# Kernel tuning notes

Measured on AMD Instinct MI355X. Metric: run time of the kernel, lower is better.

Reference implementation:

```python
import jax, jax.numpy as jnp
import numpy as np

B, N, D = 256, 512, 64  # batch, positions, channels; units = spatial_units = D


def setup_inputs() -> dict:
    key = jax.random.key(0)
    ks = jax.random.split(key, 9)
    g = 1.0 / np.sqrt(D)  # glorot-ish scale for square matrices
    return {
        "x": jax.random.normal(ks[0], (B, N, D), dtype=jnp.float32),
        "Wq_t": jax.random.normal(ks[1], (D, D), dtype=jnp.float32) * g,
        "Wk_t": jax.random.normal(ks[2], (D, D), dtype=jnp.float32) * g,
        "Wv_t": jax.random.normal(ks[3], (D, D), dtype=jnp.float32) * g,
        "Wq_s": jax.random.normal(ks[4], (D, D), dtype=jnp.float32) * g,
        "Wk_s": jax.random.normal(ks[5], (D, D), dtype=jnp.float32) * g,
        "Wv_s": jax.random.normal(ks[6], (D, D), dtype=jnp.float32) * g,
        "Wd_t": jax.random.normal(ks[7], (D, D), dtype=jnp.float32) * g,
        "bd_t": jnp.zeros((D,), dtype=jnp.float32),
        "Wd_s": jax.random.normal(ks[8], (D, D), dtype=jnp.float32) * g,
        "bd_s": jnp.zeros((D,), dtype=jnp.float32),
    }


def _branch(x, Wq, Wk, Wv, Wd, bd):
    # x: [B, N, D]; one self-attention branch followed by a Dense layer.
    q = jnp.einsum("bnd,de->bne", x, Wq)
    k = jnp.einsum("bnd,de->bne", x, Wk)
    v = jnp.einsum("bnd,de->bne", x, Wv)
    scale = 1.0 / jnp.sqrt(jnp.asarray(Wk.shape[-1], dtype=x.dtype))
    scores = jnp.einsum("bne,bme->bnm", q, k) * scale  # [B, N, N]
    w = jax.nn.softmax(scores, axis=-1)
    attn = jnp.einsum("bnm,bmd->bnd", w, v)
    return jnp.einsum("bnd,de->bne", attn, Wd) + bd


def reference(x, Wq_t, Wk_t, Wv_t, Wq_s, Wk_s, Wv_s, Wd_t, bd_t, Wd_s, bd_s):
    temporal = _branch(x, Wq_t, Wk_t, Wv_t, Wd_t, bd_t)
    spatial = _branch(x, Wq_s, Wk_s, Wv_s, Wd_s, bd_s)
    gate = jax.nn.sigmoid(temporal + spatial)
    return x * gate
```

## Files before the change

kernel.cpp:

```cpp
#include <hip/hip_runtime.h>
#include <hip/hip_bf16.h>

typedef __attribute__((ext_vector_type(8))) short short8;
typedef __attribute__((ext_vector_type(4))) short short4v;
typedef __attribute__((ext_vector_type(4))) float float4v;

#define MFMA16(a, b, c) __builtin_amdgcn_mfma_f32_16x16x32_bf16((a), (b), (c), 0, 0, 0)
#define LDS_FENCE() asm volatile("" ::: "memory")

constexpr int kN = 512;
constexpr int kD = 64;
constexpr int kThreads = 1024;

constexpr int LDS_TOTAL_BYTES = 79872 * 2;

static __device__ __forceinline__ unsigned short f2bf(float f) {
  unsigned int u = __float_as_uint(f);
  u = (u + 0x7fffu + ((u >> 16) & 1u)) >> 16;
  return (unsigned short)u;
}

static __device__ __forceinline__ unsigned int f2bf2(float a, float b) {
  union {
    __hip_bfloat162 h;
    unsigned int u;
  } cvt;
  cvt.h = __float22bfloat162_rn(float2{a, b});
  return cvt.u;
}

union S8U4 {
  short8 s8;
  unsigned int u4[4];
};

__global__ __launch_bounds__(kThreads, 4) void ts_attn_fused(
    const float* __restrict__ x, const float* __restrict__ Wq_t,
    const float* __restrict__ Wk_t, const float* __restrict__ Wv_t,
    const float* __restrict__ Wq_s, const float* __restrict__ Wk_s,
    const float* __restrict__ Wv_s, const float* __restrict__ Wd_t,
    const float* __restrict__ bd_t, const float* __restrict__ Wd_s,
    const float* __restrict__ bd_s, float* __restrict__ out) {
  extern __shared__ __align__(16) unsigned short smem_us[];
  unsigned short* Ksw = smem_us;
  unsigned short* Vsw = smem_us + 32768;
  unsigned short* Wdsw = smem_us + 65536;
  unsigned short* rep = smem_us + 69632;

  const int tid = threadIdx.x;
  const int wv = tid >> 6;
  const int lane = tid & 63;
  const int ln = lane & 15;
  const int quad = lane >> 4;
  const int b = blockIdx.x;

  const float* xb = x + (size_t)b * (kN * kD);
  float* outb = out + (size_t)b * (kN * kD);

  const int sd = tid >> 4;
  const int se0 = (tid & 15) * 4;
  const int sbase = (sd >> 3) * 512 + (sd & 7);

  float bdsum[4];
#pragma unroll
  for (int nt = 0; nt < 4; ++nt) bdsum[nt] = bd_t[nt * 16 + ln] + bd_s[nt * 16 + ln];

#pragma unroll 1
  for (int br = 0; br < 2; ++br) {
    const float* Wq = br ? Wq_s : Wq_t;
    const float* Wk = br ? Wk_s : Wk_t;
    const float* Wv = br ? Wv_s : Wv_t;
    const float* Wd = br ? Wd_s : Wd_t;

    {
      const float* srcs[3] = {Wq, Wk, Wv};
      unsigned short* dsts[3] = {rep, rep + 4096, Wdsw};
#pragma unroll
      for (int g = 0; g < 3; ++g) {
        const float4v u = *reinterpret_cast<const float4v*>(srcs[g] + sd * 64 + se0);
        unsigned short* dst = dsts[g];
#pragma unroll
        for (int i = 0; i < 4; ++i) dst[sbase + (se0 + i) * 8] = f2bf(u[i]);
      }
    }
    __syncthreads();

    short8 xa[2][2];
#pragma unroll
    for (int mi = 0; mi < 2; ++mi) {
      const int mrow = (wv + mi * 16) * 16 + ln;
      const float4v u0 = *reinterpret_cast<const float4v*>(xb + mrow * 64 + quad * 8);
      const float4v v0 = *reinterpret_cast<const float4v*>(xb + mrow * 64 + quad * 8 + 4);
      const float4v u1 = *reinterpret_cast<const float4v*>(xb + mrow * 64 + 32 + quad * 8);
      const float4v v1 = *reinterpret_cast<const float4v*>(xb + mrow * 64 + 32 + quad * 8 + 4);
      S8U4 t0, t1;
      t0.u4[0] = f2bf2(u0[0], u0[1]);
      t0.u4[1] = f2bf2(u0[2], u0[3]);
      t0.u4[2] = f2bf2(v0[0], v0[1]);
      t0.u4[3] = f2bf2(v0[2], v0[3]);
      t1.u4[0] = f2bf2(u1[0], u1[1]);
      t1.u4[1] = f2bf2(u1[2], u1[3]);
      t1.u4[2] = f2bf2(v1[0], v1[1]);
      t1.u4[3] = f2bf2(v1[2], v1[3]);
      xa[mi][0] = t0.s8;
      xa[mi][1] = t1.s8;
    }

    short4v qd[2][4];
#pragma unroll
    for (int g = 0; g < 3; ++g) {
      const unsigned short* Wl = (g == 0) ? rep : (g == 1) ? (rep + 4096) : Wdsw;
#pragma unroll
      for (int nt = 0; nt < 4; ++nt) {
        const short8 b0 = *reinterpret_cast<const short8*>(Wl + quad * 512 + (nt * 16 + ln) * 8);
        const short8 b1 =
            *reinterpret_cast<const short8*>(Wl + (4 + quad) * 512 + (nt * 16 + ln) * 8);
#pragma unroll
        for (int mi = 0; mi < 2; ++mi) {
          const int mt = wv + mi * 16;
          float4v acc = {0.f, 0.f, 0.f, 0.f};
          acc = MFMA16(xa[mi][0], b0, acc);
          acc = MFMA16(xa[mi][1], b1, acc);
          if (g == 0) {
            short4v pk;
#pragma unroll
            for (int r = 0; r < 4; ++r) pk[r] = (short)f2bf(acc[r]);
            qd[mi][nt] = pk;
          } else if (g == 1) {
            const int ehi = nt * 2 + (ln >> 3);
            const int elo = ln & 7;
#pragma unroll
            for (int r = 0; r < 4; ++r)
              Ksw[ehi * 4096 + (mt * 16 + quad * 4 + r) * 8 + elo] = f2bf(acc[r]);
          } else {
            short4v pk;
#pragma unroll
            for (int r = 0; r < 4; ++r) pk[r] = (short)f2bf(acc[r]);
            const int vbase = (mt * 2 + (quad >> 1)) * 512 + (nt * 16 + ln) * 8 + (quad & 1) * 4;
            *reinterpret_cast<short4v*>(Vsw + vbase) = pk;
          }
        }
      }
    }
    __syncthreads();

    {
      const float4v u = *reinterpret_cast<const float4v*>(Wd + sd * 64 + se0);
#pragma unroll
      for (int i = 0; i < 4; ++i) Wdsw[sbase + (se0 + i) * 8] = f2bf(u[i]);
    }
    __syncthreads();

    unsigned short* buf = rep + wv * 640;

    short8 q[2][2];
#pragma unroll
    for (int u = 0; u < 2; ++u) {
#pragma unroll
      for (int p = 0; p < 2; ++p) {
#pragma unroll
        for (int h = 0; h < 2; ++h)
#pragma unroll
          for (int r = 0; r < 4; ++r)
            buf[(quad * 4 + r) * 40 + h * 16 + ln] = (unsigned short)qd[u][p * 2 + h][r];
        LDS_FENCE();
        q[u][p] = *reinterpret_cast<const short8*>(buf + ln * 40 + quad * 8);
        LDS_FENCE();
      }
    }

    float sum[2][4];
    float4v o[2][4];
#pragma unroll
    for (int u = 0; u < 2; ++u)
#pragma unroll
      for (int i = 0; i < 4; ++i) {
        sum[u][i] = 0.f;
        o[u][i] = (float4v){0.f, 0.f, 0.f, 0.f};
      }

#pragma unroll 1
    for (int sc = 0; sc < 8; ++sc) {
      float4v s[2][4];
#pragma unroll
      for (int t = 0; t < 4; ++t) {
        const int nt = sc * 4 + t;
        const short8 k0 = *reinterpret_cast<const short8*>(Ksw + quad * 4096 + (nt * 16 + ln) * 8);
        const short8 k1 =
            *reinterpret_cast<const short8*>(Ksw + (4 + quad) * 4096 + (nt * 16 + ln) * 8);
#pragma unroll
        for (int u = 0; u < 2; ++u) {
          float4v acc = {0.f, 0.f, 0.f, 0.f};
          acc = MFMA16(q[u][0], k0, acc);
          acc = MFMA16(q[u][1], k1, acc);
          s[u][t] = acc;
        }
      }
#pragma unroll
      for (int kc2 = 0; kc2 < 2; ++kc2) {
        const int kcg = sc * 2 + kc2;
        short8 pa[2];
#pragma unroll
        for (int u = 0; u < 2; ++u) {
#pragma unroll
          for (int t2 = 0; t2 < 2; ++t2) {
            const float4v sv = s[u][kc2 * 2 + t2];
#pragma unroll
            for (int r = 0; r < 4; ++r) {
              const float p = __expf(sv[r] * 0.125f);
              sum[u][r] += p;
              buf[(quad * 4 + r) * 40 + t2 * 16 + ln] = f2bf(p);
            }
          }
          LDS_FENCE();
          pa[u] = *reinterpret_cast<const short8*>(buf + ln * 40 + quad * 8);
          LDS_FENCE();
        }
#pragma unroll
        for (int nto = 0; nto < 4; ++nto) {
          const short8 vf =
              *reinterpret_cast<const short8*>(Vsw + (kcg * 4 + quad) * 512 + (nto * 16 + ln) * 8);
          o[0][nto] = MFMA16(pa[0], vf, o[0][nto]);
          o[1][nto] = MFMA16(pa[1], vf, o[1][nto]);
        }
      }
    }

#pragma unroll
    for (int dd = 1; dd < 16; dd <<= 1)
#pragma unroll
      for (int u = 0; u < 2; ++u)
#pragma unroll
        for (int r = 0; r < 4; ++r) sum[u][r] += __shfl_xor(sum[u][r], dd, 64);
    float inv[2][4];
#pragma unroll
    for (int u = 0; u < 2; ++u)
#pragma unroll
      for (int r = 0; r < 4; ++r) inv[u][r] = 1.0f / sum[u][r];

    short8 a[2][2];
#pragma unroll
    for (int u = 0; u < 2; ++u) {
#pragma unroll
      for (int p = 0; p < 2; ++p) {
#pragma unroll
        for (int h = 0; h < 2; ++h)
#pragma unroll
          for (int r = 0; r < 4; ++r)
            buf[(quad * 4 + r) * 40 + h * 16 + ln] = f2bf(o[u][p * 2 + h][r] * inv[u][r]);
        LDS_FENCE();
        a[u][p] = *reinterpret_cast<const short8*>(buf + ln * 40 + quad * 8);
        LDS_FENCE();
      }
    }

#pragma unroll
    for (int nt = 0; nt < 4; ++nt) {
      const short8 w0 = *reinterpret_cast<const short8*>(Wdsw + quad * 512 + (nt * 16 + ln) * 8);
      const short8 w1 =
          *reinterpret_cast<const short8*>(Wdsw + (4 + quad) * 512 + (nt * 16 + ln) * 8);
      const int col = nt * 16 + ln;
#pragma unroll
      for (int u = 0; u < 2; ++u) {
        float4v d4 = {0.f, 0.f, 0.f, 0.f};
        d4 = MFMA16(a[u][0], w0, d4);
        d4 = MFMA16(a[u][1], w1, d4);
        const int m0 = (wv + u * 16) * 16 + quad * 4;
        if (br == 0) {
#pragma unroll
          for (int r = 0; r < 4; ++r) outb[(m0 + r) * 64 + col] = d4[r];
        } else {
#pragma unroll
          for (int r = 0; r < 4; ++r) {
            const float z = outb[(m0 + r) * 64 + col] + d4[r] + bdsum[nt];
            const float gate = 1.0f / (1.0f + __expf(-z));
            outb[(m0 + r) * 64 + col] = xb[(m0 + r) * 64 + col] * gate;
          }
        }
      }
    }
    __syncthreads();
  }
}

extern "C" void kernel_launch(void* const* d_in, const int* in_sizes, int n_in,
                              void* d_out, int out_size, void* d_ws, size_t ws_size,
                              hipStream_t stream) {
  const float* x = (const float*)d_in[0];
  const float* Wq_t = (const float*)d_in[1];
  const float* Wk_t = (const float*)d_in[2];
  const float* Wv_t = (const float*)d_in[3];
  const float* Wq_s = (const float*)d_in[4];
  const float* Wk_s = (const float*)d_in[5];
  const float* Wv_s = (const float*)d_in[6];
  const float* Wd_t = (const float*)d_in[7];
  const float* bd_t = (const float*)d_in[8];
  const float* Wd_s = (const float*)d_in[9];
  const float* bd_s = (const float*)d_in[10];
  float* out = (float*)d_out;

  hipFuncSetAttribute(reinterpret_cast<const void*>(ts_attn_fused),
                      hipFuncAttributeMaxDynamicSharedMemorySize, LDS_TOTAL_BYTES);
  ts_attn_fused<<<dim3(256), dim3(kThreads), LDS_TOTAL_BYTES, stream>>>(
      x, Wq_t, Wk_t, Wv_t, Wq_s, Wk_s, Wv_s, Wd_t, bd_t, Wd_s, bd_s, out);
}
```

Before: 211.5 us.

## Halve block to 8 waves, each computing four query tiles with shared K/V fragments

The block drops from 16 to 8 waves, so each wave now owns four 16-row query tiles instead of two. Each K and V fragment read from LDS is reused across twice as many MFMAs, which cuts LDS read traffic per unit of work. The per-wave staging buffer becomes two slots so that transposes can be batched, and the x-load is moved ahead of the barrier. In exchange, register pressure roughly doubles for the accumulators and there is less parallelism per block, with launch bounds lowered to match.

```diff
diff --git a/kernel.cpp b/kernel.cpp
--- a/kernel.cpp
+++ b/kernel.cpp
@@ -10,7 +10,7 @@
 
 constexpr int kN = 512;
 constexpr int kD = 64;
-constexpr int kThreads = 1024;
+constexpr int kThreads = 512;
 
 constexpr int LDS_TOTAL_BYTES = 79872 * 2;
 
@@ -34,7 +34,7 @@
   unsigned int u4[4];
 };
 
-__global__ __launch_bounds__(kThreads, 4) void ts_attn_fused(
+__global__ __launch_bounds__(kThreads, 2) void ts_attn_fused(
     const float* __restrict__ x, const float* __restrict__ Wq_t,
     const float* __restrict__ Wk_t, const float* __restrict__ Wv_t,
     const float* __restrict__ Wq_s, const float* __restrict__ Wk_s,
@@ -57,13 +57,16 @@
   const float* xb = x + (size_t)b * (kN * kD);
   float* outb = out + (size_t)b * (kN * kD);
 
-  const int sd = tid >> 4;
-  const int se0 = (tid & 15) * 4;
+  const int sd = tid >> 3;
+  const int se0 = (tid & 7) * 8;
   const int sbase = (sd >> 3) * 512 + (sd & 7);
 
   float bdsum[4];
 #pragma unroll
   for (int nt = 0; nt < 4; ++nt) bdsum[nt] = bd_t[nt * 16 + ln] + bd_s[nt * 16 + ln];
+
+  unsigned short* slot0 = rep + wv * 1280;
+  unsigned short* slot1 = slot0 + 640;
 
 #pragma unroll 1
   for (int br = 0; br < 2; ++br) {
@@ -77,18 +80,20 @@
       unsigned short* dsts[3] = {rep, rep + 4096, Wdsw};
 #pragma unroll
       for (int g = 0; g < 3; ++g) {
-        const float4v u = *reinterpret_cast<const float4v*>(srcs[g] + sd * 64 + se0);
+        const float4v u0 = *reinterpret_cast<const float4v*>(srcs[g] + sd * 64 + se0);
+        const float4v u1 = *reinterpret_cast<const float4v*>(srcs[g] + sd * 64 + se0 + 4);
         unsigned short* dst = dsts[g];
 #pragma unroll
-        for (int i = 0; i < 4; ++i) dst[sbase + (se0 + i) * 8] = f2bf(u[i]);
-      }
-    }
-    __syncthreads();
-
-    short8 xa[2][2];
-#pragma unroll
-    for (int mi = 0; mi < 2; ++mi) {
-      const int mrow = (wv + mi * 16) * 16 + ln;
+        for (int i = 0; i < 4; ++i) dst[sbase + (se0 + i) * 8] = f2bf(u0[i]);
+#pragma unroll
+        for (int i = 0; i < 4; ++i) dst[sbase + (se0 + 4 + i) * 8] = f2bf(u1[i]);
+      }
+    }
+
+    short8 xa[4][2];
+#pragma unroll
+    for (int mi = 0; mi < 4; ++mi) {
+      const int mrow = (wv + mi * 8) * 16 + ln;
       const float4v u0 = *reinterpret_cast<const float4v*>(xb + mrow * 64 + quad * 8);
       const float4v v0 = *reinterpret_cast<const float4v*>(xb + mrow * 64 + quad * 8 + 4);
       const float4v u1 = *reinterpret_cast<const float4v*>(xb + mrow * 64 + 32 + quad * 8);
@@ -105,8 +110,9 @@
       xa[mi][0] = t0.s8;
       xa[mi][1] = t1.s8;
     }
-
-    short4v qd[2][4];
+    __syncthreads();
+
+    short4v qd[4][4];
 #pragma unroll
     for (int g = 0; g < 3; ++g) {
       const unsigned short* Wl = (g == 0) ? rep : (g == 1) ? (rep + 4096) : Wdsw;
@@ -116,8 +122,8 @@
         const short8 b1 =
             *reinterpret_cast<const short8*>(Wl + (4 + quad) * 512 + (nt * 16 + ln) * 8);
 #pragma unroll
-        for (int mi = 0; mi < 2; ++mi) {
-          const int mt = wv + mi * 16;
+        for (int mi = 0; mi < 4; ++mi) {
+          const int mt = wv + mi * 8;
           float4v acc = {0.f, 0.f, 0.f, 0.f};
           acc = MFMA16(xa[mi][0], b0, acc);
           acc = MFMA16(xa[mi][1], b1, acc);
@@ -145,34 +151,35 @@
     __syncthreads();
 
     {
-      const float4v u = *reinterpret_cast<const float4v*>(Wd + sd * 64 + se0);
-#pragma unroll
-      for (int i = 0; i < 4; ++i) Wdsw[sbase + (se0 + i) * 8] = f2bf(u[i]);
+      const float4v u0 = *reinterpret_cast<const float4v*>(Wd + sd * 64 + se0);
+      const float4v u1 = *reinterpret_cast<const float4v*>(Wd + sd * 64 + se0 + 4);
+#pragma unroll
+      for (int i = 0; i < 4; ++i) Wdsw[sbase + (se0 + i) * 8] = f2bf(u0[i]);
+#pragma unroll
+      for (int i = 0; i < 4; ++i) Wdsw[sbase + (se0 + 4 + i) * 8] = f2bf(u1[i]);
     }
     __syncthreads();
 
-    unsigned short* buf = rep + wv * 640;
-
-    short8 q[2][2];
-#pragma unroll
-    for (int u = 0; u < 2; ++u) {
-#pragma unroll
-      for (int p = 0; p < 2; ++p) {
-#pragma unroll
-        for (int h = 0; h < 2; ++h)
-#pragma unroll
-          for (int r = 0; r < 4; ++r)
-            buf[(quad * 4 + r) * 40 + h * 16 + ln] = (unsigned short)qd[u][p * 2 + h][r];
-        LDS_FENCE();
-        q[u][p] = *reinterpret_cast<const short8*>(buf + ln * 40 + quad * 8);
-        LDS_FENCE();
-      }
-    }
-
-    float sum[2][4];
-    float4v o[2][4];
-#pragma unroll
-    for (int u = 0; u < 2; ++u)
+    short8 q[4][2];
+#pragma unroll
+    for (int u = 0; u < 4; ++u) {
+#pragma unroll
+      for (int r = 0; r < 4; ++r) {
+        slot0[(quad * 4 + r) * 40 + ln] = (unsigned short)qd[u][0][r];
+        slot0[(quad * 4 + r) * 40 + 16 + ln] = (unsigned short)qd[u][1][r];
+        slot1[(quad * 4 + r) * 40 + ln] = (unsigned short)qd[u][2][r];
+        slot1[(quad * 4 + r) * 40 + 16 + ln] = (unsigned short)qd[u][3][r];
+      }
+      LDS_FENCE();
+      q[u][0] = *reinterpret_cast<const short8*>(slot0 + ln * 40 + quad * 8);
+      q[u][1] = *reinterpret_cast<const short8*>(slot1 + ln * 40 + quad * 8);
+      LDS_FENCE();
+    }
+
+    float sum[4][4];
+    float4v o[4][4];
+#pragma unroll
+    for (int u = 0; u < 4; ++u)
 #pragma unroll
       for (int i = 0; i < 4; ++i) {
         sum[u][i] = 0.f;
@@ -180,78 +187,99 @@
       }
 
 #pragma unroll 1
-    for (int sc = 0; sc < 8; ++sc) {
-      float4v s[2][4];
-#pragma unroll
-      for (int t = 0; t < 4; ++t) {
-        const int nt = sc * 4 + t;
+    for (int kcg = 0; kcg < 16; ++kcg) {
+      float4v s[4][2];
+#pragma unroll
+      for (int h = 0; h < 2; ++h) {
+        const int nt = kcg * 2 + h;
         const short8 k0 = *reinterpret_cast<const short8*>(Ksw + quad * 4096 + (nt * 16 + ln) * 8);
         const short8 k1 =
             *reinterpret_cast<const short8*>(Ksw + (4 + quad) * 4096 + (nt * 16 + ln) * 8);
 #pragma unroll
-        for (int u = 0; u < 2; ++u) {
+        for (int u = 0; u < 4; ++u) {
           float4v acc = {0.f, 0.f, 0.f, 0.f};
           acc = MFMA16(q[u][0], k0, acc);
           acc = MFMA16(q[u][1], k1, acc);
-          s[u][t] = acc;
+          s[u][h] = acc;
         }
       }
-#pragma unroll
-      for (int kc2 = 0; kc2 < 2; ++kc2) {
-        const int kcg = sc * 2 + kc2;
-        short8 pa[2];
-#pragma unroll
-        for (int u = 0; u < 2; ++u) {
-#pragma unroll
-          for (int t2 = 0; t2 < 2; ++t2) {
-            const float4v sv = s[u][kc2 * 2 + t2];
-#pragma unroll
-            for (int r = 0; r < 4; ++r) {
-              const float p = __expf(sv[r] * 0.125f);
-              sum[u][r] += p;
-              buf[(quad * 4 + r) * 40 + t2 * 16 + ln] = f2bf(p);
-            }
+
+#pragma unroll
+      for (int u = 0; u < 2; ++u) {
+        unsigned short* sl = u ? slot1 : slot0;
+#pragma unroll
+        for (int h = 0; h < 2; ++h)
+#pragma unroll
+          for (int r = 0; r < 4; ++r) {
+            const float p = __expf(s[u][h][r] * 0.125f);
+            sum[u][r] += p;
+            sl[(quad * 4 + r) * 40 + h * 16 + ln] = f2bf(p);
           }
-          LDS_FENCE();
-          pa[u] = *reinterpret_cast<const short8*>(buf + ln * 40 + quad * 8);
-          LDS_FENCE();
-        }
-#pragma unroll
-        for (int nto = 0; nto < 4; ++nto) {
-          const short8 vf =
-              *reinterpret_cast<const short8*>(Vsw + (kcg * 4 + quad) * 512 + (nto * 16 + ln) * 8);
-          o[0][nto] = MFMA16(pa[0], vf, o[0][nto]);
-          o[1][nto] = MFMA16(pa[1], vf, o[1][nto]);
-        }
-      }
+      }
+      LDS_FENCE();
+      const short8 pa0 = *reinterpret_cast<const short8*>(slot0 + ln * 40 + quad * 8);
+      const short8 pa1 = *reinterpret_cast<const short8*>(slot1 + ln * 40 + quad * 8);
+      short8 vf[4];
+#pragma unroll
+      for (int nto = 0; nto < 4; ++nto)
+        vf[nto] =
+            *reinterpret_cast<const short8*>(Vsw + (kcg * 4 + quad) * 512 + (nto * 16 + ln) * 8);
+#pragma unroll
+      for (int nto = 0; nto < 4; ++nto) {
+        o[0][nto] = MFMA16(pa0, vf[nto], o[0][nto]);
+        o[1][nto] = MFMA16(pa1, vf[nto], o[1][nto]);
+      }
+      LDS_FENCE();
+
+#pragma unroll
+      for (int u = 2; u < 4; ++u) {
+        unsigned short* sl = (u == 3) ? slot1 : slot0;
+#pragma unroll
+        for (int h = 0; h < 2; ++h)
+#pragma unroll
+          for (int r = 0; r < 4; ++r) {
+            const float p = __expf(s[u][h][r] * 0.125f);
+            sum[u][r] += p;
+            sl[(quad * 4 + r) * 40 + h * 16 + ln] = f2bf(p);
+          }
+      }
+      LDS_FENCE();
+      const short8 pa2 = *reinterpret_cast<const short8*>(slot0 + ln * 40 + quad * 8);
+      const short8 pa3 = *reinterpret_cast<const short8*>(slot1 + ln * 40 + quad * 8);
+#pragma unroll
+      for (int nto = 0; nto < 4; ++nto) {
+        o[2][nto] = MFMA16(pa2, vf[nto], o[2][nto]);
+        o[3][nto] = MFMA16(pa3, vf[nto], o[3][nto]);
+      }
+      LDS_FENCE();
     }
 
 #pragma unroll
     for (int dd = 1; dd < 16; dd <<= 1)
 #pragma unroll
-      for (int u = 0; u < 2; ++u)
+      for (int u = 0; u < 4; ++u)
 #pragma unroll
         for (int r = 0; r < 4; ++r) sum[u][r] += __shfl_xor(sum[u][r], dd, 64);
-    float inv[2][4];
-#pragma unroll
-    for (int u = 0; u < 2; ++u)
+    float inv[4][4];
+#pragma unroll
+    for (int u = 0; u < 4; ++u)
 #pragma unroll
       for (int r = 0; r < 4; ++r) inv[u][r] = 1.0f / sum[u][r];
 
-    short8 a[2][2];
-#pragma unroll
-    for (int u = 0; u < 2; ++u) {
-#pragma unroll
-      for (int p = 0; p < 2; ++p) {
-#pragma unroll
-        for (int h = 0; h < 2; ++h)
-#pragma unroll
-          for (int r = 0; r < 4; ++r)
-            buf[(quad * 4 + r) * 40 + h * 16 + ln] = f2bf(o[u][p * 2 + h][r] * inv[u][r]);
-        LDS_FENCE();
-        a[u][p] = *reinterpret_cast<const short8*>(buf + ln * 40 + quad * 8);
-        LDS_FENCE();
-      }
+    short8 a[4][2];
+#pragma unroll
+    for (int u = 0; u < 4; ++u) {
+#pragma unroll
+      for (int r = 0; r < 4; ++r) {
+        slot0[(quad * 4 + r) * 40 + ln] = f2bf(o[u][0][r] * inv[u][r]);
+        slot0[(quad * 4 + r) * 40 + 16 + ln] = f2bf(o[u][1][r] * inv[u][r]);
+        slot1[(quad * 4 + r) * 40 + ln] = f2bf(o[u][2][r] * inv[u][r]);
+        slot1[(quad * 4 + r) * 40 + 16 + ln] = f2bf(o[u][3][r] * inv[u][r]);
+      }
+      LDS_FENCE();
+      a[u][0] = *reinterpret_cast<const short8*>(slot0 + ln * 40 + quad * 8);
+      a[u][1] = *reinterpret_cast<const short8*>(slot1 + ln * 40 + quad * 8);
+      LDS_FENCE();
     }
 
 #pragma unroll
@@ -261,11 +289,11 @@
           *reinterpret_cast<const short8*>(Wdsw + (4 + quad) * 512 + (nt * 16 + ln) * 8);
       const int col = nt * 16 + ln;
 #pragma unroll
-      for (int u = 0; u < 2; ++u) {
+      for (int u = 0; u < 4; ++u) {
         float4v d4 = {0.f, 0.f, 0.f, 0.f};
         d4 = MFMA16(a[u][0], w0, d4);
         d4 = MFMA16(a[u][1], w1, d4);
-        const int m0 = (wv + u * 16) * 16 + quad * 4;
+        const int m0 = (wv + u * 8) * 16 + quad * 4;
         if (br == 0) {
 #pragma unroll
           for (int r = 0; r < 4; ++r) outb[(m0 + r) * 64 + col] = d4[r];
```

New measurement: 250.0 us. 1.18x slower.
